# Optimization experiments

Measured on AMD Instinct MI355X. Metric: run time of the kernel, lower is better.

The kernel has to match this reference:

```python
import jax, jax.numpy as jnp
import numpy as np

H = 32      # n_heads
KV = 8      # n_kv_heads
HD = 64     # head_dim = dim // n_heads


def setup_inputs() -> dict:
    key = jax.random.key(0)
    ks = jax.random.split(key, 8)
    B, S, D = 4, 1024, 2048
    x = jax.random.normal(ks[0], (B, S, D), dtype=jnp.float32)
    # RoPE tables stored as cos/sin parts of the complex freqs_cis (seqlen, head_dim//2)
    pos = jnp.arange(S, dtype=jnp.float32)[:, None]
    inv = 1.0 / (10000.0 ** (jnp.arange(0, HD, 2, dtype=jnp.float32) / HD))[None, :]
    ang = pos * inv                          # (S, HD//2)
    freqs_cos = jnp.cos(ang)
    freqs_sin = jnp.sin(ang)
    # additive causal mask (S, S): 0 on/below diagonal, -inf above
    mask = jnp.where(jnp.tril(jnp.ones((S, S), dtype=bool)), 0.0, -jnp.inf).astype(jnp.float32)
    sc = 0.02
    wq = jax.random.normal(ks[1], (H * HD, D), dtype=jnp.float32) * sc
    wk = jax.random.normal(ks[2], (KV * HD, D), dtype=jnp.float32) * sc
    wv = jax.random.normal(ks[3], (KV * HD, D), dtype=jnp.float32) * sc
    wo = jax.random.normal(ks[4], (D, D), dtype=jnp.float32) * sc
    return {"x": x, "freqs_cos": freqs_cos, "freqs_sin": freqs_sin, "mask": mask,
            "wq": wq, "wk": wk, "wv": wv, "wo": wo}


def _rope(t, cos, sin):
    # t: (B, S, nh, HD). Faithful to source: rotation is indexed by x.shape[2]
    # (the HEAD axis, due to pre-transpose call), broadcast over sequence.
    nh = t.shape[2]
    c = cos[:nh][None, None, :, :]           # (1,1,nh,HD//2)
    s = sin[:nh][None, None, :, :]
    tr = t.reshape(*t.shape[:-1], HD // 2, 2)
    t0, t1 = tr[..., 0], tr[..., 1]
    o0 = t0 * c - t1 * s
    o1 = t0 * s + t1 * c
    return jnp.stack([o0, o1], axis=-1).reshape(t.shape)


def reference(x, freqs_cos, freqs_sin, mask, wq, wk, wv, wo):
    B, S, D = x.shape
    xq = (x @ wq.T).reshape(B, S, H, HD)
    xk = (x @ wk.T).reshape(B, S, KV, HD)
    xv = (x @ wv.T).reshape(B, S, KV, HD)
    xq = _rope(xq, freqs_cos, freqs_sin)
    xk = _rope(xk, freqs_cos, freqs_sin)
    rep = H // KV
    xk = jnp.repeat(xk, rep, axis=2)         # GQA repeat_interleave on head axis
    xv = jnp.repeat(xv, rep, axis=2)
    q = xq.transpose(0, 2, 1, 3)             # (B,H,S,HD)
    k = xk.transpose(0, 2, 1, 3)
    v = xv.transpose(0, 2, 1, 3)
    scores = jnp.einsum('bhqd,bhkd->bhqk', q, k) / np.sqrt(HD).astype(np.float32)
    scores = scores + mask[None, None, :, :]
    p = jax.nn.softmax(scores.astype(jnp.float32), axis=-1).astype(q.dtype)
    out = jnp.einsum('bhqk,bhkd->bhqd', p, v)
    out = out.transpose(0, 2, 1, 3).reshape(B, S, H * HD)
    return out @ wo.T
```

## Files before the change

kernel.cpp:

```cpp
#include <hip/hip_runtime.h>
#include <hip/hip_bf16.h>

constexpr int kB  = 4;
constexpr int kS  = 1024;
constexpr int kD  = 2048;
constexpr int kH  = 32;
constexpr int kKV = 8;
constexpr int kHD = 64;

constexpr float kNegBig = -30000.0f;
constexpr float kC = 0.125f * 1.44269504f;
constexpr float kDeferThr = 40.0f;

typedef __attribute__((ext_vector_type(8))) short short8;
typedef __attribute__((ext_vector_type(4))) float floatx4;

static __device__ __forceinline__ float bf2f(short v) {
    unsigned int u = ((unsigned int)(unsigned short)v) << 16;
    return __builtin_bit_cast(float, u);
}
static __device__ __forceinline__ short f2bf(float f) {
    unsigned int u = __builtin_bit_cast(unsigned int, f);
    unsigned int lsb = (u >> 16) & 1u;
    u += 0x7fffu + lsb;
    return (short)(u >> 16);
}
static __device__ __forceinline__ short f2bf_fast(float f) {
    unsigned int u = __builtin_bit_cast(unsigned int, f);
    return (short)((u + 0x8000u) >> 16);
}

static __device__ __forceinline__ void load_lds16(const short* g, short* l) {
    __builtin_amdgcn_global_load_lds(
        (const __attribute__((address_space(1))) unsigned int*)g,
        (__attribute__((address_space(3))) unsigned int*)l, 16, 0, 0);
}

__global__ void cast_f2b(const float* __restrict__ in, short* __restrict__ outp, int n4) {
    int gid = blockIdx.x * blockDim.x + threadIdx.x;
    if (gid >= n4) return;
    float4 v = ((const float4*)in)[gid];
    short4 o;
    o.x = f2bf(v.x); o.y = f2bf(v.y); o.z = f2bf(v.z); o.w = f2bf(v.w);
    ((short4*)outp)[gid] = o;
}

template <typename OT, int ROPE>
__global__ __launch_bounds__(256) void gemm_bt_lds(const short* __restrict__ A,
                                                   const short* __restrict__ Bm,
                                                   OT* __restrict__ C,
                                                   int M, int N, int K,
                                                   const float* __restrict__ cosb,
                                                   const float* __restrict__ sinb) {
    __shared__ short As[128 * 32];
    __shared__ short Bs[128 * 32];

    int tid  = threadIdx.x;
    int wave = tid >> 6, lane = tid & 63;
    int quad = lane >> 4, l16 = lane & 15;
    int wm = wave >> 1, wn = wave & 1;

    int nwg  = gridDim.x * gridDim.y;
    int orig = blockIdx.y * gridDim.x + blockIdx.x;
    int wg   = orig;
    if ((nwg & 7) == 0) {
        int cpx = nwg >> 3;
        wg = (orig & 7) * cpx + (orig >> 3);
    }
    int bx = wg % gridDim.x, by = wg / gridDim.x;
    int m0 = by * 128, n0 = bx * 128;

    floatx4 acc[4][4];
    for (int i = 0; i < 4; i++)
        for (int j = 0; j < 4; j++) acc[i][j] = (floatx4){0.f, 0.f, 0.f, 0.f};

    int srow = lane >> 2;
    int skc  = (lane & 3) * 8;

    for (int k0 = 0; k0 < K; k0 += 32) {
        __syncthreads();
        for (int i = 0; i < 2; i++) {
            int r16 = wave * 32 + i * 16;
            load_lds16(A + (long)(m0 + r16 + srow) * K + k0 + skc, &As[r16 * 32]);
            load_lds16(Bm + (long)(n0 + r16 + srow) * K + k0 + skc, &Bs[r16 * 32]);
        }
        __syncthreads();

        short8 af[4], bfr[4];
        for (int i = 0; i < 4; i++)
            af[i] = *(const short8*)&As[(wm * 64 + i * 16 + l16) * 32 + quad * 8];
        for (int j = 0; j < 4; j++)
            bfr[j] = *(const short8*)&Bs[(wn * 64 + j * 16 + l16) * 32 + quad * 8];
        for (int i = 0; i < 4; i++)
            for (int j = 0; j < 4; j++)
                acc[i][j] = __builtin_amdgcn_mfma_f32_16x16x32_bf16(
                    af[i], bfr[j], acc[i][j], 0, 0, 0);
    }

    for (int j = 0; j < 4; j++) {
        int col = n0 + wn * 64 + j * 16 + l16;
        float c = 0.f, s = 0.f;
        bool rope_col = (ROPE == 1) || (ROPE == 2 && col < 512);
        if constexpr (ROPE != 0) {
            if (rope_col) {
                int hh = col >> 6;
                int ii = (col & 63) >> 1;
                c = cosb[hh * 32 + ii];
                s = sinb[hh * 32 + ii];
            }
        }
        for (int i = 0; i < 4; i++) {
            for (int r = 0; r < 4; r++) {
                int row = m0 + wm * 64 + i * 16 + quad * 4 + r;
                float v = acc[i][j][r];
                if constexpr (ROPE != 0) {
                    float p = __shfl_xor(v, 1);
                    if (rope_col)
                        v = (col & 1) ? (p * s + v * c)
                                      : (v * c - p * s);
                }
                if constexpr (sizeof(OT) == 2)
                    C[(long)row * N + col] = f2bf(v);
                else
                    C[(long)row * N + col] = v;
            }
        }
    }
}

__global__ __launch_bounds__(512) void attn_kernel(const short* __restrict__ xq,
                                                   const short* __restrict__ xk,
                                                   const short* __restrict__ xv,
                                                   short* __restrict__ out,
                                                   int kvstride) {
    __shared__ short vT[64][72];
    __shared__ short pT[8][16][72];

    int qt = gridDim.x - 1 - blockIdx.x;
    int h = blockIdx.y, b = blockIdx.z;
    int kvh = h >> 2;
    int tid = threadIdx.x, wave = tid >> 6, lane = tid & 63;
    int quad = lane >> 4, l16 = lane & 15;

    int wr0  = qt * 128 + wave * 16;
    int wr1  = wr0 + 15;
    int qrow = wr0 + l16;
    int crow = wr0 + quad * 4;

    const short* qp = xq + (((long)b * kS + qrow) * kH + h) * kHD + quad * 8;
    short8 qf0 = *(const short8*)(qp);
    short8 qf1 = *(const short8*)(qp + 32);

    short8 ones;
    for (int i = 0; i < 8; i++) ones[i] = (short)0x3F80;

    float m_run[4];
    floatx4 acc_l = (floatx4){0.f, 0.f, 0.f, 0.f};
    floatx4 acc_o[4];
    for (int r = 0; r < 4; r++) m_run[r] = kNegBig;
    for (int nb = 0; nb < 4; nb++) acc_o[nb] = (floatx4){0.f, 0.f, 0.f, 0.f};

    int vkey = tid & 63;
    int vdb  = wave * 8;
    const short* vbase = xv + (long)b * kS * kvstride + kvh * kHD;

    short8 vr = *(const short8*)(vbase + (long)vkey * kvstride + vdb);

    const short* kbase0 = xk + (long)b * kS * kvstride + kvh * kHD;
    int nt = 2 * qt + 2;

    for (int kt = 0; kt < nt; kt++) {
        bool wactive = (kt * 64 <= wr1);

        short8 kf[4][2];
        if (wactive) {
            const short* kbase = kbase0 + (long)kt * 64 * kvstride;
            for (int kb = 0; kb < 4; kb++) {
                const short* kp = kbase + (long)(kb * 16 + l16) * kvstride + quad * 8;
                kf[kb][0] = *(const short8*)kp;
                kf[kb][1] = *(const short8*)(kp + 32);
            }
        }

        __syncthreads();
        for (int i = 0; i < 8; i++)
            vT[vdb + i][vkey] = vr[i];
        if (kt + 1 < nt) {
            vr = *(const short8*)(vbase + (long)((kt + 1) * 64 + vkey) * kvstride + vdb);
        }
        __syncthreads();

        if (!wactive) continue;

        floatx4 accs[4];
        __builtin_amdgcn_s_setprio(1);
        for (int kb = 0; kb < 4; kb++) {
            accs[kb] = (floatx4){0.f, 0.f, 0.f, 0.f};
            accs[kb] = __builtin_amdgcn_mfma_f32_16x16x32_bf16(qf0, kf[kb][0], accs[kb], 0, 0, 0);
            accs[kb] = __builtin_amdgcn_mfma_f32_16x16x32_bf16(qf1, kf[kb][1], accs[kb], 0, 0, 0);
        }
        __builtin_amdgcn_s_setprio(0);

        float sv[4][4];
        for (int kb = 0; kb < 4; kb++)
            for (int r = 0; r < 4; r++) sv[r][kb] = accs[kb][r];

        if (kt * 64 + 63 > wr0) {
            for (int kb = 0; kb < 4; kb++)
                for (int r = 0; r < 4; r++) {
                    int kj = kt * 64 + kb * 16 + l16;
                    if (kj > crow + r) sv[r][kb] = kNegBig;
                }
        }

        float mx[4];
        for (int r = 0; r < 4; r++) {
            float m1 = fmaxf(fmaxf(sv[r][0], sv[r][1]), fmaxf(sv[r][2], sv[r][3]));
            for (int off = 1; off < 16; off <<= 1) m1 = fmaxf(m1, __shfl_xor(m1, off));
            mx[r] = m1;
        }
        bool small = (mx[0] - m_run[0] <= kDeferThr) && (mx[1] - m_run[1] <= kDeferThr) &&
                     (mx[2] - m_run[2] <= kDeferThr) && (mx[3] - m_run[3] <= kDeferThr);
        if (!__all(small)) {
            for (int r = 0; r < 4; r++) {
                float mnew = fmaxf(m_run[r], mx[r]);
                float alpha = exp2f((m_run[r] - mnew) * kC);
                m_run[r] = mnew;
                acc_l[r] *= alpha;
                for (int nb = 0; nb < 4; nb++) acc_o[nb][r] *= alpha;
            }
        }

        for (int r = 0; r < 4; r++) {
            float mk = m_run[r] * kC;
            for (int kb = 0; kb < 4; kb++)
                sv[r][kb] = exp2f(fmaf(sv[r][kb], kC, -mk));
        }

        for (int r = 0; r < 4; r++)
            for (int kb = 0; kb < 4; kb++)
                pT[wave][quad * 4 + r][kb * 16 + l16] = f2bf_fast(sv[r][kb]);

        short8 pf0 = *(const short8*)&pT[wave][l16][quad * 8];
        short8 pf1 = *(const short8*)&pT[wave][l16][32 + quad * 8];
        __builtin_amdgcn_s_setprio(1);
        acc_l = __builtin_amdgcn_mfma_f32_16x16x32_bf16(pf0, ones, acc_l, 0, 0, 0);
        acc_l = __builtin_amdgcn_mfma_f32_16x16x32_bf16(pf1, ones, acc_l, 0, 0, 0);
        for (int nb = 0; nb < 4; nb++) {
            short8 vf0 = *(const short8*)&vT[nb * 16 + l16][quad * 8];
            short8 vf1 = *(const short8*)&vT[nb * 16 + l16][32 + quad * 8];
            acc_o[nb] = __builtin_amdgcn_mfma_f32_16x16x32_bf16(pf0, vf0, acc_o[nb], 0, 0, 0);
            acc_o[nb] = __builtin_amdgcn_mfma_f32_16x16x32_bf16(pf1, vf1, acc_o[nb], 0, 0, 0);
        }
        __builtin_amdgcn_s_setprio(0);
    }

    for (int r = 0; r < 4; r++) {
        float inv = 1.0f / fmaxf(acc_l[r], 1e-20f);
        int row = crow + r;
        for (int nb = 0; nb < 4; nb++)
            out[(((long)b * kS + row) * kH + h) * kHD + nb * 16 + l16] =
                f2bf(acc_o[nb][r] * inv);
    }
}

extern "C" void kernel_launch(void* const* d_in, const int* in_sizes, int n_in,
                              void* d_out, int out_size, void* d_ws, size_t ws_size,
                              hipStream_t stream) {
    const float* x  = (const float*)d_in[0];
    const float* fc = (const float*)d_in[1];
    const float* fs = (const float*)d_in[2];
    const float* wq = (const float*)d_in[4];
    const float* wk = (const float*)d_in[5];
    const float* wv = (const float*)d_in[6];
    const float* wo = (const float*)d_in[7];

    const int M = kB * kS;
    const long MB = 1l << 20;

    char* ws = (char*)d_ws;
    short* xb   = (short*)(ws);
    short* wqb  = (short*)(ws + 16 * MB);
    short* wkvb = (short*)(ws + 16 * MB);
    short* ao   = (short*)(ws);
    short* wob  = (short*)(ws + 16 * MB);
    char*  dob  = (char*)d_out;
    short* xq   = (short*)(dob);
    short* xkv  = (short*)(dob + 16 * MB);

    const int nX  = M * kD;
    const int nWq = kD * kD;
    const int nWk = kKV * kHD * kD;

    cast_f2b<<<(nX / 4 + 255) / 256, 256, 0, stream>>>(x, xb, nX / 4);
    cast_f2b<<<(nWq / 4 + 255) / 256, 256, 0, stream>>>(wq, wqb, nWq / 4);
    gemm_bt_lds<short, 1><<<dim3(kD / 128, M / 128), 256, 0, stream>>>(
        xb, wqb, xq, M, kD, kD, fc, fs);

    cast_f2b<<<(nWk / 4 + 255) / 256, 256, 0, stream>>>(wk, wkvb, nWk / 4);
    cast_f2b<<<(nWk / 4 + 255) / 256, 256, 0, stream>>>(wv, wkvb + nWk, nWk / 4);
    gemm_bt_lds<short, 2><<<dim3(1024 / 128, M / 128), 256, 0, stream>>>(
        xb, wkvb, xkv, M, 1024, kD, fc, fs);

    attn_kernel<<<dim3(kS / 128, kH, kB), 512, 0, stream>>>(
        xq, xkv, xkv + 512, ao, 1024);

    cast_f2b<<<(nWq / 4 + 255) / 256, 256, 0, stream>>>(wo, wob, nWq / 4);
    gemm_bt_lds<float, 0><<<dim3(kD / 128, M / 128), 256, 0, stream>>>(
        ao, wob, (float*)d_out, M, kD, kD, nullptr, nullptr);
}
```

Baseline: 422.6 us.

## Write V transposed from KV GEMM epilogue and load it directly in attention

The KV projection GEMM epilogue now writes V in a transposed (dim-major) layout into a separate buffer. The attention kernel reads V fragments straight from global memory instead of staging and transposing them through LDS, which removes two barriers per key tile. The attention block also shrinks from 8 to 4 waves (64 query rows), giving twice as many blocks and removing idle waves on the diagonal tiles. The cost is strided short4 stores in the GEMM epilogue and uncoalesced, cache-dependent V reads in the inner loop.

```diff
diff --git a/kernel.cpp b/kernel.cpp
--- a/kernel.cpp
+++ b/kernel.cpp
@@ -51,7 +51,8 @@
                                                    OT* __restrict__ C,
                                                    int M, int N, int K,
                                                    const float* __restrict__ cosb,
-                                                   const float* __restrict__ sinb) {
+                                                   const float* __restrict__ sinb,
+                                                   short* __restrict__ Vt) {
     __shared__ short As[128 * 32];
     __shared__ short Bs[128 * 32];
 
@@ -99,6 +100,23 @@
 
     for (int j = 0; j < 4; j++) {
         int col = n0 + wn * 64 + j * 16 + l16;
+
+        if constexpr (ROPE == 2) {
+            if (col >= 512) {
+                int cv = col - 512;
+                for (int i = 0; i < 4; i++) {
+                    int row0 = m0 + wm * 64 + i * 16 + quad * 4;
+                    short4 o;
+                    o.x = f2bf(acc[i][j][0]);
+                    o.y = f2bf(acc[i][j][1]);
+                    o.z = f2bf(acc[i][j][2]);
+                    o.w = f2bf(acc[i][j][3]);
+                    *(short4*)&Vt[(long)cv * M + row0] = o;
+                }
+                continue;
+            }
+        }
+
         float c = 0.f, s = 0.f;
         bool rope_col = (ROPE == 1) || (ROPE == 2 && col < 512);
         if constexpr (ROPE != 0) {
@@ -128,22 +146,20 @@
     }
 }
 
-__global__ __launch_bounds__(512) void attn_kernel(const short* __restrict__ xq,
+__global__ __launch_bounds__(256) void attn_kernel(const short* __restrict__ xq,
                                                    const short* __restrict__ xk,
-                                                   const short* __restrict__ xv,
+                                                   const short* __restrict__ vt,
                                                    short* __restrict__ out,
                                                    int kvstride) {
-    __shared__ short vT[64][72];
-    __shared__ short pT[8][16][72];
-
-    int qt = gridDim.x - 1 - blockIdx.x;
+    __shared__ short pT[4][16][72];
+
+    int qb = gridDim.x - 1 - blockIdx.x;
     int h = blockIdx.y, b = blockIdx.z;
     int kvh = h >> 2;
     int tid = threadIdx.x, wave = tid >> 6, lane = tid & 63;
     int quad = lane >> 4, l16 = lane & 15;
 
-    int wr0  = qt * 128 + wave * 16;
-    int wr1  = wr0 + 15;
+    int wr0  = qb * 64 + wave * 16;
     int qrow = wr0 + l16;
     int crow = wr0 + quad * 4;
 
@@ -160,37 +176,19 @@
     for (int r = 0; r < 4; r++) m_run[r] = kNegBig;
     for (int nb = 0; nb < 4; nb++) acc_o[nb] = (floatx4){0.f, 0.f, 0.f, 0.f};
 
-    int vkey = tid & 63;
-    int vdb  = wave * 8;
-    const short* vbase = xv + (long)b * kS * kvstride + kvh * kHD;
-
-    short8 vr = *(const short8*)(vbase + (long)vkey * kvstride + vdb);
-
     const short* kbase0 = xk + (long)b * kS * kvstride + kvh * kHD;
-    int nt = 2 * qt + 2;
+    const short* vbase = vt + (long)kvh * kHD * (kB * kS) + (long)b * kS;
+
+    int nt = qb + 1;
 
     for (int kt = 0; kt < nt; kt++) {
-        bool wactive = (kt * 64 <= wr1);
-
         short8 kf[4][2];
-        if (wactive) {
-            const short* kbase = kbase0 + (long)kt * 64 * kvstride;
-            for (int kb = 0; kb < 4; kb++) {
-                const short* kp = kbase + (long)(kb * 16 + l16) * kvstride + quad * 8;
-                kf[kb][0] = *(const short8*)kp;
-                kf[kb][1] = *(const short8*)(kp + 32);
-            }
-        }
-
-        __syncthreads();
-        for (int i = 0; i < 8; i++)
-            vT[vdb + i][vkey] = vr[i];
-        if (kt + 1 < nt) {
-            vr = *(const short8*)(vbase + (long)((kt + 1) * 64 + vkey) * kvstride + vdb);
-        }
-        __syncthreads();
-
-        if (!wactive) continue;
+        const short* kbase = kbase0 + (long)kt * 64 * kvstride;
+        for (int kb = 0; kb < 4; kb++) {
+            const short* kp = kbase + (long)(kb * 16 + l16) * kvstride + quad * 8;
+            kf[kb][0] = *(const short8*)kp;
+            kf[kb][1] = *(const short8*)(kp + 32);
+        }
 
         floatx4 accs[4];
         __builtin_amdgcn_s_setprio(1);
@@ -205,7 +203,7 @@
         for (int kb = 0; kb < 4; kb++)
             for (int r = 0; r < 4; r++) sv[r][kb] = accs[kb][r];
 
-        if (kt * 64 + 63 > wr0) {
+        if (kt == nt - 1) {
             for (int kb = 0; kb < 4; kb++)
                 for (int r = 0; r < 4; r++) {
                     int kj = kt * 64 + kb * 16 + l16;
@@ -241,16 +239,21 @@
             for (int kb = 0; kb < 4; kb++)
                 pT[wave][quad * 4 + r][kb * 16 + l16] = f2bf_fast(sv[r][kb]);
 
+        short8 vf[4][2];
+        for (int nb = 0; nb < 4; nb++) {
+            const short* vp = vbase + (long)(nb * 16 + l16) * (kB * kS) + kt * 64 + quad * 8;
+            vf[nb][0] = *(const short8*)(vp);
+            vf[nb][1] = *(const short8*)(vp + 32);
+        }
+
         short8 pf0 = *(const short8*)&pT[wave][l16][quad * 8];
         short8 pf1 = *(const short8*)&pT[wave][l16][32 + quad * 8];
         __builtin_amdgcn_s_setprio(1);
         acc_l = __builtin_amdgcn_mfma_f32_16x16x32_bf16(pf0, ones, acc_l, 0, 0, 0);
         acc_l = __builtin_amdgcn_mfma_f32_16x16x32_bf16(pf1, ones, acc_l, 0, 0, 0);
         for (int nb = 0; nb < 4; nb++) {
-            short8 vf0 = *(const short8*)&vT[nb * 16 + l16][quad * 8];
-            short8 vf1 = *(const short8*)&vT[nb * 16 + l16][32 + quad * 8];
-            acc_o[nb] = __builtin_amdgcn_mfma_f32_16x16x32_bf16(pf0, vf0, acc_o[nb], 0, 0, 0);
-            acc_o[nb] = __builtin_amdgcn_mfma_f32_16x16x32_bf16(pf1, vf1, acc_o[nb], 0, 0, 0);
+            acc_o[nb] = __builtin_amdgcn_mfma_f32_16x16x32_bf16(pf0, vf[nb][0], acc_o[nb], 0, 0, 0);
+            acc_o[nb] = __builtin_amdgcn_mfma_f32_16x16x32_bf16(pf1, vf[nb][1], acc_o[nb], 0, 0, 0);
         }
         __builtin_amdgcn_s_setprio(0);
     }
@@ -287,6 +290,7 @@
     char*  dob  = (char*)d_out;
     short* xq   = (short*)(dob);
     short* xkv  = (short*)(dob + 16 * MB);
+    short* vt   = (short*)(dob + 24 * MB);
 
     const int nX  = M * kD;
     const int nWq = kD * kD;
@@ -295,17 +299,17 @@
     cast_f2b<<<(nX / 4 + 255) / 256, 256, 0, stream>>>(x, xb, nX / 4);
     cast_f2b<<<(nWq / 4 + 255) / 256, 256, 0, stream>>>(wq, wqb, nWq / 4);
     gemm_bt_lds<short, 1><<<dim3(kD / 128, M / 128), 256, 0, stream>>>(
-        xb, wqb, xq, M, kD, kD, fc, fs);
+        xb, wqb, xq, M, kD, kD, fc, fs, nullptr);
 
     cast_f2b<<<(nWk / 4 + 255) / 256, 256, 0, stream>>>(wk, wkvb, nWk / 4);
     cast_f2b<<<(nWk / 4 + 255) / 256, 256, 0, stream>>>(wv, wkvb + nWk, nWk / 4);
     gemm_bt_lds<short, 2><<<dim3(1024 / 128, M / 128), 256, 0, stream>>>(
-        xb, wkvb, xkv, M, 1024, kD, fc, fs);
-
-    attn_kernel<<<dim3(kS / 128, kH, kB), 512, 0, stream>>>(
-        xq, xkv, xkv + 512, ao, 1024);
+        xb, wkvb, xkv, M, 1024, kD, fc, fs, vt);
+
+    attn_kernel<<<dim3(kS / 64, kH, kB), 256, 0, stream>>>(
+        xq, xkv, vt, ao, 1024);
 
     cast_f2b<<<(nWq / 4 + 255) / 256, 256, 0, stream>>>(wo, wob, nWq / 4);
     gemm_bt_lds<float, 0><<<dim3(kD / 128, M / 128), 256, 0, stream>>>(
-        ao, wob, (float*)d_out, M, kD, kD, nullptr, nullptr);
-}
+        ao, wob, (float*)d_out, M, kD, kD, nullptr, nullptr, nullptr);
+}
```

New measurement: 513.3 us. 1.21x slower.
